# Performance work log

Hardware: AMD Instinct MI355X
Metric: run time of the kernel (lower is better)

## Reference

```python
import jax, jax.numpy as jnp
import numpy as np


def _splat(img, sx, sy, w):
    """One bilinear-gaussian corner splat (scatter-add).
    img: (N,C,H,W); sx,sy,w: (N,1,H,W) integer-valued float shifts + weight.
    Returns (img_warp, one_warp) each (N,C,H,W).
    """
    N, C, H, W = img.shape
    ix = sx.astype(jnp.int32) + jnp.arange(H, dtype=jnp.int32)[None, None, :, None]
    iy = sy.astype(jnp.int32) + jnp.arange(W, dtype=jnp.int32)[None, None, None, :]
    mask = (ix >= 0) & (ix < H) & (iy >= 0) & (iy < W)          # (N,1,H,W)
    ixc = jnp.clip(ix, 0, H - 1)
    iyc = jnp.clip(iy, 0, W - 1)
    nb = jnp.arange(N, dtype=jnp.int32)[:, None, None, None]
    cb = jnp.arange(C, dtype=jnp.int32)[None, :, None, None]
    ids = ((nb * C + cb) * H + ixc) * W + iyc                   # (N,C,H,W)
    ids = jnp.broadcast_to(ids, (N, C, H, W)).reshape(-1)
    wv = jnp.where(mask, w, 0.0)                                # invalid -> 0 contribution
    vals = jnp.broadcast_to(img * wv, (N, C, H, W)).reshape(-1)
    wflat = jnp.broadcast_to(wv, (N, C, H, W)).reshape(-1)
    img_warp = jnp.zeros(N * C * H * W, img.dtype).at[ids].add(vals)
    one_warp = jnp.zeros(N * C * H * W, img.dtype).at[ids].add(wflat)
    return img_warp.reshape(N, C, H, W), one_warp.reshape(N, C, H, W)


def setup_inputs() -> dict:
    key = jax.random.key(0)
    k1, k2 = jax.random.split(key)
    N, C, H, W = 4, 128, 216, 384
    img = jax.random.normal(k1, (N, C, H, W), dtype=jnp.float32)
    # flow displacements of a few pixels magnitude (realistic optical flow)
    flo = jax.random.normal(k2, (N, 2, H, W), dtype=jnp.float32) * 8.0
    return {"img": img, "flo": flo}


def reference(img, flo):
    # y shifts rows (H axis), x shifts cols (W axis), matching the torch code
    y = flo[:, 0:1]    # (N,1,H,W)
    x = flo[:, 1:2]
    x1 = jnp.floor(x); x2 = x1 + 1.0
    y1 = jnp.floor(y); y2 = y1 + 1.0
    w11 = jnp.exp(-((x - x1) ** 2 + (y - y1) ** 2))
    w12 = jnp.exp(-((x - x1) ** 2 + (y - y2) ** 2))
    w21 = jnp.exp(-((x - x2) ** 2 + (y - y1) ** 2))
    w22 = jnp.exp(-((x - x2) ** 2 + (y - y2) ** 2))
    img11, o11 = _splat(img, x1, y1, w11)
    img12, o12 = _splat(img, x1, y2, w12)
    img21, o21 = _splat(img, x2, y1, w21)
    img22, o22 = _splat(img, x2, y2, w22)
    imgw = img11 + img12 + img21 + img22
    o = o11 + o12 + o21 + o22
    return imgw, o
```

## Files before the change

kernel.cpp:

```cpp
#include <hip/hip_runtime.h>


constexpr int N_ = 4, C_ = 128, H_ = 216, W_ = 384;
constexpr int HW    = H_ * W_;
constexpr int TOTAL = N_ * C_ * HW;
constexpr int PIX   = N_ * HW;
constexpr int SCAN_BLOCKS = PIX / 256;
constexpr int PTILE = 64;
constexpr int GATHER_BLOCKS = PIX / PTILE;

constexpr size_t OFF_IMGT   = 0;
constexpr size_t OFF_COUNTS = (size_t)TOTAL;
constexpr size_t OFF_CURSOR = OFF_COUNTS + PIX;
constexpr size_t OFF_OFFS   = OFF_CURSOR + PIX;
constexpr size_t OFF_BS     = OFF_OFFS + PIX;
constexpr size_t OFF_ENT    = OFF_BS + 4096;
constexpr size_t WS_ELEMS   = OFF_ENT + 8ull * PIX;
constexpr size_t WS_BYTES   = WS_ELEMS * 4;

__device__ inline void corner_math(float fx, float fy, int& ifx, int& ify,
                                   float& ex0, float& ex1, float& ey0, float& ey1) {
    float fx1 = floorf(fx), fy1 = floorf(fy);
    float dx = fx - fx1, dy = fy - fy1;
    ifx = (int)fx1; ify = (int)fy1;
    ex0 = __expf(-dx * dx);
    ex1 = __expf(-(dx - 1.f) * (dx - 1.f));
    ey0 = __expf(-dy * dy);
    ey1 = __expf(-(dy - 1.f) * (dy - 1.f));
}

__global__ __launch_bounds__(256) void transpose_fwd_k(const float* __restrict__ img,
                                                       float* __restrict__ imgT) {
    __shared__ float tile[32][33];
    int n   = blockIdx.z;
    int hw0 = blockIdx.x * 32;
    int c0  = blockIdx.y * 32;
    const float* src = img  + (size_t)n * C_ * HW;
    float*       dst = imgT + (size_t)n * HW * C_;
    int tx = threadIdx.x, ty = threadIdx.y;
#pragma unroll
    for (int r = 0; r < 32; r += 8)
        tile[ty + r][tx] = src[(size_t)(c0 + ty + r) * HW + hw0 + tx];
    __syncthreads();
#pragma unroll
    for (int r = 0; r < 32; r += 8)
        dst[(size_t)(hw0 + ty + r) * C_ + c0 + tx] = tile[tx][ty + r];
}

__global__ __launch_bounds__(256) void count_k(const float* __restrict__ flo,
                                               unsigned int* __restrict__ counts) {
    int idx = blockIdx.x * 256 + threadIdx.x;
    if (idx >= PIX) return;
    int s = idx % HW, n = idx / HW;
    int h = s / W_, w = s % W_;
    float fy = flo[(n * 2 + 0) * HW + s];
    float fx = flo[(n * 2 + 1) * HW + s];
    int ifx, ify; float ex0, ex1, ey0, ey1;
    corner_math(fx, fy, ifx, ify, ex0, ex1, ey0, ey1);
    int ix = h + ifx, iy = w + ify;
    unsigned int* base = counts + (size_t)n * HW;
    bool bx0 = (unsigned)ix       < (unsigned)H_;
    bool bx1 = (unsigned)(ix + 1) < (unsigned)H_;
    bool by0 = (unsigned)iy       < (unsigned)W_;
    bool by1 = (unsigned)(iy + 1) < (unsigned)W_;
    if (bx0 && by0) atomicAdd(base + ix * W_ + iy, 1u);
    if (bx0 && by1) atomicAdd(base + ix * W_ + iy + 1, 1u);
    if (bx1 && by0) atomicAdd(base + (ix + 1) * W_ + iy, 1u);
    if (bx1 && by1) atomicAdd(base + (ix + 1) * W_ + iy + 1, 1u);
}

__global__ __launch_bounds__(256) void scan_local_k(const unsigned int* __restrict__ counts,
                                                    unsigned int* __restrict__ offs,
                                                    unsigned int* __restrict__ bs) {
    __shared__ unsigned int tmp[256];
    int tid = threadIdx.x;
    int i = blockIdx.x * 256 + tid;
    unsigned int v = counts[i];
    tmp[tid] = v;
    __syncthreads();
    for (int off = 1; off < 256; off <<= 1) {
        unsigned int t = (tid >= off) ? tmp[tid - off] : 0u;
        __syncthreads();
        tmp[tid] += t;
        __syncthreads();
    }
    offs[i] = tmp[tid] - v;
    if (tid == 255) bs[blockIdx.x] = tmp[tid];
}

__global__ __launch_bounds__(256) void scan_bs_k(unsigned int* __restrict__ bs) {
    __shared__ unsigned int tmp[256];
    constexpr int IT = 6;
    int tid = threadIdx.x;
    unsigned int v[IT]; unsigned int sum = 0;
#pragma unroll
    for (int i = 0; i < IT; ++i) {
        int j = tid * IT + i;
        v[i] = (j < SCAN_BLOCKS) ? bs[j] : 0u;
        sum += v[i];
    }
    tmp[tid] = sum;
    __syncthreads();
    for (int off = 1; off < 256; off <<= 1) {
        unsigned int t = (tid >= off) ? tmp[tid - off] : 0u;
        __syncthreads();
        tmp[tid] += t;
        __syncthreads();
    }
    unsigned int run = tmp[tid] - sum;
#pragma unroll
    for (int i = 0; i < IT; ++i) {
        int j = tid * IT + i;
        if (j < SCAN_BLOCKS) { unsigned int old = v[i]; bs[j] = run; run += old; }
    }
}

__global__ __launch_bounds__(256) void fill_k(const float* __restrict__ flo,
                                              const unsigned int* __restrict__ offs,
                                              const unsigned int* __restrict__ bs,
                                              unsigned int* __restrict__ cursor,
                                              uint2* __restrict__ entries) {
    int idx = blockIdx.x * 256 + threadIdx.x;
    if (idx >= PIX) return;
    int s = idx % HW, n = idx / HW;
    int h = s / W_, w = s % W_;
    float fy = flo[(n * 2 + 0) * HW + s];
    float fx = flo[(n * 2 + 1) * HW + s];
    int ifx, ify; float ex0, ex1, ey0, ey1;
    corner_math(fx, fy, ifx, ify, ex0, ex1, ey0, ey1);
    int ix = h + ifx, iy = w + ify;
    bool bx[2] = { (unsigned)ix < (unsigned)H_, (unsigned)(ix + 1) < (unsigned)H_ };
    bool by[2] = { (unsigned)iy < (unsigned)W_, (unsigned)(iy + 1) < (unsigned)W_ };
    float exw[2] = { ex0, ex1 }, eyw[2] = { ey0, ey1 };
#pragma unroll
    for (int a = 0; a < 2; ++a) {
#pragma unroll
        for (int b = 0; b < 2; ++b) {
            if (bx[a] && by[b]) {
                int t = n * HW + (ix + a) * W_ + (iy + b);
                unsigned int slot = atomicAdd(cursor + t, 1u);
                unsigned int e = offs[t] + bs[t >> 8] + slot;
                entries[e] = make_uint2((unsigned int)s,
                                        __float_as_uint(exw[a] * eyw[b]));
            }
        }
    }
}

__global__ __launch_bounds__(256) void gather_fused_k(const float* __restrict__ imgT,
                                                      const unsigned int* __restrict__ counts,
                                                      const unsigned int* __restrict__ offs,
                                                      const unsigned int* __restrict__ bs,
                                                      const uint2* __restrict__ entries,
                                                      float* __restrict__ out_img,
                                                      float* __restrict__ out_ones) {
    __shared__ float tile[C_ * PTILE];
    __shared__ float wsum_lds[PTILE];

    int tid = threadIdx.x;
    int pl  = tid >> 5;
    int cg  = tid & 31;
    int bt  = blockIdx.x;
    int n   = bt / (HW / PTILE);
    int p0  = (bt % (HW / PTILE)) * PTILE;
    const float4* srcBase = (const float4*)(imgT + (size_t)n * HW * C_);

    float4 acc[8];
    float  ws[8];
#pragma unroll
    for (int si = 0; si < 8; ++si) {
        int p = si * 8 + pl;
        int t = n * HW + p0 + p;
        unsigned int k   = counts[t];
        unsigned int off = offs[t] + bs[t >> 8];
        float4 a = make_float4(0.f, 0.f, 0.f, 0.f);
        float  w_s = 0.f;
        unsigned int j = 0;
        for (; j + 2 <= k; j += 2) {
            uint2 e0 = entries[off + j];
            uint2 e1 = entries[off + j + 1];
            float w0 = __uint_as_float(e0.y);
            float w1 = __uint_as_float(e1.y);
            float4 v0 = srcBase[(size_t)e0.x * (C_ / 4) + cg];
            float4 v1 = srcBase[(size_t)e1.x * (C_ / 4) + cg];
            a.x = a.x + w0 * v0.x + w1 * v1.x;
            a.y = a.y + w0 * v0.y + w1 * v1.y;
            a.z = a.z + w0 * v0.z + w1 * v1.z;
            a.w = a.w + w0 * v0.w + w1 * v1.w;
            w_s = w_s + w0 + w1;
        }
        if (j < k) {
            uint2 e0 = entries[off + j];
            float w0 = __uint_as_float(e0.y);
            float4 v0 = srcBase[(size_t)e0.x * (C_ / 4) + cg];
            a.x += w0 * v0.x; a.y += w0 * v0.y;
            a.z += w0 * v0.z; a.w += w0 * v0.w;
            w_s += w0;
        }
        acc[si] = a; ws[si] = w_s;
    }

#pragma unroll
    for (int si = 0; si < 8; ++si) {
        int p  = si * 8 + pl;
        if (cg == 0) wsum_lds[p] = ws[si];
        int p4 = p >> 2, pr = p & 3;
        float av[4] = { acc[si].x, acc[si].y, acc[si].z, acc[si].w };
#pragma unroll
        for (int jj = 0; jj < 4; ++jj) {
            int c    = 4 * cg + jj;
            int slot = p4 ^ ((c >> 2) & 15);
            tile[c * PTILE + slot * 4 + pr] = av[jj];
        }
    }
    __syncthreads();

    int p4    = tid & 15;
    int cbase = tid >> 4;
    float4 wv = ((const float4*)wsum_lds)[p4];
#pragma unroll
    for (int i = 0; i < 8; ++i) {
        int c    = cbase + 16 * i;
        int slot = p4 ^ ((c >> 2) & 15);
        float4 v = *(const float4*)&tile[c * PTILE + slot * 4];
        size_t o = ((size_t)(n * C_ + c)) * HW + p0 + p4 * 4;
        *(float4*)(out_img  + o) = v;
        *(float4*)(out_ones + o) = wv;
    }
}

__global__ __launch_bounds__(256) void fb_ones_scatter_k(const float* __restrict__ flo,
                                                         float* __restrict__ out_ones) {
    int idx = blockIdx.x * 256 + threadIdx.x;
    if (idx >= PIX) return;
    int w = idx % W_; int hn = idx / W_; int h = hn % H_; int n = hn / H_;
    float fy = flo[(n * 2 + 0) * HW + h * W_ + w];
    float fx = flo[(n * 2 + 1) * HW + h * W_ + w];
    int ifx, ify; float ex0, ex1, ey0, ey1;
    corner_math(fx, fy, ifx, ify, ex0, ex1, ey0, ey1);
    int ix = h + ifx, iy = w + ify;
    float* plane = out_ones + (size_t)n * C_ * HW;
    if ((unsigned)ix < (unsigned)H_ && (unsigned)iy < (unsigned)W_) atomicAdd(plane + ix * W_ + iy, ex0 * ey0);
    if ((unsigned)ix < (unsigned)H_ && (unsigned)(iy+1) < (unsigned)W_) atomicAdd(plane + ix * W_ + iy + 1, ex0 * ey1);
    if ((unsigned)(ix+1) < (unsigned)H_ && (unsigned)iy < (unsigned)W_) atomicAdd(plane + (ix+1) * W_ + iy, ex1 * ey0);
    if ((unsigned)(ix+1) < (unsigned)H_ && (unsigned)(iy+1) < (unsigned)W_) atomicAdd(plane + (ix+1) * W_ + iy + 1, ex1 * ey1);
}

__global__ __launch_bounds__(256) void fb_img_scatter_k(const float* __restrict__ img,
                                                        const float* __restrict__ flo,
                                                        float* __restrict__ out_img) {
    int idx = blockIdx.x * 256 + threadIdx.x;
    if (idx >= TOTAL) return;
    int w = idx % W_; int rem = idx / W_; int h = rem % H_; rem /= H_;
    int c = rem % C_; int n = rem / C_;
    float fy = flo[(n * 2 + 0) * HW + h * W_ + w];
    float fx = flo[(n * 2 + 1) * HW + h * W_ + w];
    int ifx, ify; float ex0, ex1, ey0, ey1;
    corner_math(fx, fy, ifx, ify, ex0, ex1, ey0, ey1);
    int ix = h + ifx, iy = w + ify;
    float v = img[idx];
    float* plane = out_img + (size_t)(n * C_ + c) * HW;
    if ((unsigned)ix < (unsigned)H_ && (unsigned)iy < (unsigned)W_) atomicAdd(plane + ix * W_ + iy, v * ex0 * ey0);
    if ((unsigned)ix < (unsigned)H_ && (unsigned)(iy+1) < (unsigned)W_) atomicAdd(plane + ix * W_ + iy + 1, v * ex0 * ey1);
    if ((unsigned)(ix+1) < (unsigned)H_ && (unsigned)iy < (unsigned)W_) atomicAdd(plane + (ix+1) * W_ + iy, v * ex1 * ey0);
    if ((unsigned)(ix+1) < (unsigned)H_ && (unsigned)(iy+1) < (unsigned)W_) atomicAdd(plane + (ix+1) * W_ + iy + 1, v * ex1 * ey1);
}

__global__ __launch_bounds__(256) void fb_ones_bcast_k(float* __restrict__ out_ones) {
    constexpr int HW4 = HW / 4;
    constexpr int TOT = N_ * (C_ - 1) * HW4;
    int idx = blockIdx.x * 256 + threadIdx.x;
    if (idx >= TOT) return;
    int p = idx % HW4; int cn = idx / HW4;
    int c = 1 + cn % (C_ - 1); int n = cn / (C_ - 1);
    const float4* src = (const float4*)(out_ones + (size_t)n * C_ * HW);
    float4*       dst = (float4*)(out_ones + ((size_t)n * C_ + c) * HW);
    dst[p] = src[p];
}

extern "C" void kernel_launch(void* const* d_in, const int* in_sizes, int n_in,
                              void* d_out, int out_size, void* d_ws, size_t ws_size,
                              hipStream_t stream) {
    const float* img = (const float*)d_in[0];
    const float* flo = (const float*)d_in[1];
    float* out      = (float*)d_out;
    float* out_img  = out;
    float* out_ones = out + (size_t)TOTAL;

    if (ws_size < WS_BYTES) {
        hipMemsetAsync(out_img, 0, (size_t)TOTAL * sizeof(float), stream);
        for (int n = 0; n < N_; ++n)
            hipMemsetAsync(out_ones + (size_t)n * C_ * HW, 0, HW * sizeof(float), stream);
        fb_ones_scatter_k<<<(PIX + 255) / 256, 256, 0, stream>>>(flo, out_ones);
        fb_img_scatter_k<<<(TOTAL + 255) / 256, 256, 0, stream>>>(img, flo, out_img);
        fb_ones_bcast_k<<<(N_ * (C_ - 1) * (HW / 4) + 255) / 256, 256, 0, stream>>>(out_ones);
        return;
    }

    float* ws = (float*)d_ws;
    float*        imgT    = ws + OFF_IMGT;
    unsigned int* counts  = (unsigned int*)(ws + OFF_COUNTS);
    unsigned int* cursor  = (unsigned int*)(ws + OFF_CURSOR);
    unsigned int* offs    = (unsigned int*)(ws + OFF_OFFS);
    unsigned int* bs      = (unsigned int*)(ws + OFF_BS);
    uint2*        entries = (uint2*)(ws + OFF_ENT);

    hipMemsetAsync(counts, 0, 2ull * PIX * sizeof(unsigned int), stream);

    dim3 tb(32, 8);
    transpose_fwd_k<<<dim3(HW / 32, C_ / 32, N_), tb, 0, stream>>>(img, imgT);
    count_k<<<SCAN_BLOCKS, 256, 0, stream>>>(flo, counts);
    scan_local_k<<<SCAN_BLOCKS, 256, 0, stream>>>(counts, offs, bs);
    scan_bs_k<<<1, 256, 0, stream>>>(bs);
    fill_k<<<SCAN_BLOCKS, 256, 0, stream>>>(flo, offs, bs, cursor, entries);
    gather_fused_k<<<GATHER_BLOCKS, 256, 0, stream>>>(imgT, counts, offs, bs,
                                                      entries, out_img, out_ones);
}
```

Measured before the change: 762.6 us.

## Balance gather work by splitting each tile's entry range evenly across warps

The gather kernel no longer gives each 32-lane group a fixed set of 8 destination pixels with uneven entry counts. It now stages the tile's contiguous entry range into LDS in chunks and splits it evenly across the 8 groups. Each entry carries its local pixel index in the high bits of the source index. Per-pixel partial sums are flushed into the LDS tile with shared-memory atomics whenever the pixel changes. This is meant to remove load imbalance and warp divergence from variable splat counts, at the cost of extra LDS atomics, tile zeroing, chunk staging and block-wide barriers.

```diff
diff --git a/kernel.cpp b/kernel.cpp
--- a/kernel.cpp
+++ b/kernel.cpp
@@ -8,6 +8,7 @@
 constexpr int SCAN_BLOCKS = PIX / 256;
 constexpr int PTILE = 64;
 constexpr int GATHER_BLOCKS = PIX / PTILE;
+constexpr int ECHUNK = 512;
 
 constexpr size_t OFF_IMGT   = 0;
 constexpr size_t OFF_COUNTS = (size_t)TOTAL;
@@ -140,7 +141,7 @@
                 int t = n * HW + (ix + a) * W_ + (iy + b);
                 unsigned int slot = atomicAdd(cursor + t, 1u);
                 unsigned int e = offs[t] + bs[t >> 8] + slot;
-                entries[e] = make_uint2((unsigned int)s,
+                entries[e] = make_uint2((unsigned int)s | ((unsigned int)(t & 63) << 20),
                                         __float_as_uint(exw[a] * eyw[b]));
             }
         }
@@ -156,63 +157,80 @@
                                                       float* __restrict__ out_ones) {
     __shared__ float tile[C_ * PTILE];
     __shared__ float wsum_lds[PTILE];
+    __shared__ uint2 ent_lds[ECHUNK];
 
     int tid = threadIdx.x;
-    int pl  = tid >> 5;
+    int g   = tid >> 5;
     int cg  = tid & 31;
     int bt  = blockIdx.x;
     int n   = bt / (HW / PTILE);
     int p0  = (bt % (HW / PTILE)) * PTILE;
     const float4* srcBase = (const float4*)(imgT + (size_t)n * HW * C_);
 
-    float4 acc[8];
-    float  ws[8];
-#pragma unroll
-    for (int si = 0; si < 8; ++si) {
-        int p = si * 8 + pl;
-        int t = n * HW + p0 + p;
-        unsigned int k   = counts[t];
-        unsigned int off = offs[t] + bs[t >> 8];
-        float4 a = make_float4(0.f, 0.f, 0.f, 0.f);
-        float  w_s = 0.f;
-        unsigned int j = 0;
-        for (; j + 2 <= k; j += 2) {
-            uint2 e0 = entries[off + j];
-            uint2 e1 = entries[off + j + 1];
-            float w0 = __uint_as_float(e0.y);
-            float w1 = __uint_as_float(e1.y);
-            float4 v0 = srcBase[(size_t)e0.x * (C_ / 4) + cg];
-            float4 v1 = srcBase[(size_t)e1.x * (C_ / 4) + cg];
-            a.x = a.x + w0 * v0.x + w1 * v1.x;
-            a.y = a.y + w0 * v0.y + w1 * v1.y;
-            a.z = a.z + w0 * v0.z + w1 * v1.z;
-            a.w = a.w + w0 * v0.w + w1 * v1.w;
-            w_s = w_s + w0 + w1;
+    {
+        float4 z = make_float4(0.f, 0.f, 0.f, 0.f);
+        float4* t4 = (float4*)tile;
+#pragma unroll
+        for (int i = 0; i < 8; ++i) t4[tid + 256 * i] = z;
+        if (tid < 16) ((float4*)wsum_lds)[tid] = z;
+    }
+
+    int t0 = n * HW + p0;
+    int t63 = t0 + 63;
+    unsigned int E_base = offs[t0]  + bs[t0 >> 8];
+    unsigned int E_end  = offs[t63] + bs[t63 >> 8] + counts[t63];
+
+    float4 acc = make_float4(0.f, 0.f, 0.f, 0.f);
+    float  wacc = 0.f;
+    int    cur_p = -1;
+
+    auto flush = [&]() {
+        if (cur_p >= 0) {
+            int p4 = cur_p >> 2, pr = cur_p & 3;
+            int basei = (p4 ^ (cg & 15)) * 4 + pr;
+            atomicAdd(&tile[(4 * cg + 0) * PTILE + basei], acc.x);
+            atomicAdd(&tile[(4 * cg + 1) * PTILE + basei], acc.y);
+            atomicAdd(&tile[(4 * cg + 2) * PTILE + basei], acc.z);
+            atomicAdd(&tile[(4 * cg + 3) * PTILE + basei], acc.w);
+            if (cg == 0) atomicAdd(&wsum_lds[cur_p], wacc);
         }
-        if (j < k) {
-            uint2 e0 = entries[off + j];
-            float w0 = __uint_as_float(e0.y);
-            float4 v0 = srcBase[(size_t)e0.x * (C_ / 4) + cg];
-            a.x += w0 * v0.x; a.y += w0 * v0.y;
-            a.z += w0 * v0.z; a.w += w0 * v0.w;
-            w_s += w0;
+        acc = make_float4(0.f, 0.f, 0.f, 0.f);
+        wacc = 0.f;
+    };
+
+#define PROC(E, V)                                            \
+    {                                                         \
+        int p_ = (int)((E).x >> 20);                          \
+        if (p_ != cur_p) { flush(); cur_p = p_; }             \
+        float w_ = __uint_as_float((E).y);                    \
+        acc.x += w_ * (V).x; acc.y += w_ * (V).y;             \
+        acc.z += w_ * (V).z; acc.w += w_ * (V).w;             \
+        wacc  += w_;                                          \
+    }
+
+    for (unsigned int cb = E_base; cb < E_end; cb += ECHUNK) {
+        unsigned int m  = min((unsigned int)ECHUNK, E_end - cb);
+        unsigned int mp = (m + 31u) & ~31u;
+        __syncthreads();
+        for (unsigned int i = tid; i < mp; i += 256)
+            ent_lds[i] = (i < m) ? entries[cb + i] : make_uint2(0u, 0u);
+        __syncthreads();
+        unsigned int span = mp >> 3;
+        unsigned int b = g * span;
+        for (unsigned int i = 0; i < span; i += 4) {
+            uint2 E0 = ent_lds[b + i + 0];
+            uint2 E1 = ent_lds[b + i + 1];
+            uint2 E2 = ent_lds[b + i + 2];
+            uint2 E3 = ent_lds[b + i + 3];
+            float4 V0 = srcBase[(size_t)(E0.x & 0xFFFFFu) * (C_ / 4) + cg];
+            float4 V1 = srcBase[(size_t)(E1.x & 0xFFFFFu) * (C_ / 4) + cg];
+            float4 V2 = srcBase[(size_t)(E2.x & 0xFFFFFu) * (C_ / 4) + cg];
+            float4 V3 = srcBase[(size_t)(E3.x & 0xFFFFFu) * (C_ / 4) + cg];
+            PROC(E0, V0); PROC(E1, V1); PROC(E2, V2); PROC(E3, V3);
         }
-        acc[si] = a; ws[si] = w_s;
-    }
-
-#pragma unroll
-    for (int si = 0; si < 8; ++si) {
-        int p  = si * 8 + pl;
-        if (cg == 0) wsum_lds[p] = ws[si];
-        int p4 = p >> 2, pr = p & 3;
-        float av[4] = { acc[si].x, acc[si].y, acc[si].z, acc[si].w };
-#pragma unroll
-        for (int jj = 0; jj < 4; ++jj) {
-            int c    = 4 * cg + jj;
-            int slot = p4 ^ ((c >> 2) & 15);
-            tile[c * PTILE + slot * 4 + pr] = av[jj];
-        }
-    }
+    }
+    flush();
+#undef PROC
     __syncthreads();
 
     int p4    = tid & 15;
```

Measured after the change: 798.9 us. +4.8%, slower.
